# Optimization experiments

Hardware: AMD Instinct MI355X
Metric: run time of the kernel (lower is better)

The kernel has to match this reference:

```python
import jax, jax.numpy as jnp
import numpy as np

NB_HEAD = 12
INPUT_DIM = 768
HEAD_DIM = INPUT_DIM // NB_HEAD


def setup_inputs() -> dict:
    key = jax.random.key(0)
    kx, kq, kv = jax.random.split(key, 3)
    x = jax.random.normal(kx, (32, 512, INPUT_DIM), dtype=jnp.float32)
    # per-head params stacked on a leading head axis; original init: uniform(-0.1, 0.1)
    Q = jax.random.uniform(kq, (NB_HEAD, INPUT_DIM, INPUT_DIM), dtype=jnp.float32, minval=-0.1, maxval=0.1)
    V = jax.random.uniform(kv, (NB_HEAD, INPUT_DIM, HEAD_DIM), dtype=jnp.float32, minval=-0.1, maxval=0.1)
    return {"x": x, "Q": Q, "V": V}


def reference(x, Q, V):
    # x: [b, n, d]; Q: [h, d, d]; V: [h, d, e] with e = head_dim
    b, n, d = x.shape
    h = Q.shape[0]
    q = jnp.einsum('bnd,hde->bhne', x, Q)            # per-head query proj
    scores = jnp.einsum('bhne,bme->bhnm', q, x)      # QK^T with raw x as keys (no scaling)
    att = jax.nn.softmax(scores, axis=-1)            # softmax over keys
    weighted = jnp.einsum('bhnm,bmd->bhnd', att, x)  # attention-weighted values (raw x)
    out = jnp.einsum('bhnd,hde->bhne', weighted, V)  # per-head output proj
    # concat heads along feature dim (head 0 first, matching torch.cat)
    return out.transpose(0, 2, 1, 3).reshape(b, n, h * V.shape[-1])
```

## Files before the change

kernel.cpp:

```cpp
#include <hip/hip_runtime.h>
#include <stdint.h>

#define B_SZ 32
#define SEQ  512
#define DIM  768
#define NH   12
#define HD   64
#define ROWS (B_SZ*SEQ)

typedef __attribute__((ext_vector_type(4))) float f32x4;
typedef __attribute__((ext_vector_type(8))) _Float16 half8;

#define GLOAD_LDS16(gaddr, laddr) \
  __builtin_amdgcn_global_load_lds((const __attribute__((address_space(1))) void*)(gaddr), \
                                   (__attribute__((address_space(3))) void*)(laddr), 16, 0, 0)

__device__ __forceinline__ unsigned short h2u(_Float16 h){
  union { _Float16 h; unsigned short u; } c; c.h = h; return c.u;
}
__device__ __forceinline__ unsigned short f2hu(float f){
  return h2u((_Float16)f);
}

__global__ void k_split(const float* __restrict__ x,
                        unsigned short* __restrict__ xh,
                        unsigned short* __restrict__ xl, int n4){
  int i = blockIdx.x * 256 + threadIdx.x;
  if (i >= n4) return;
  float4 v = ((const float4*)x)[i];
  ushort4 h, l;
  _Float16 t;
  t = (_Float16)v.x; h.x = h2u(t); l.x = f2hu(v.x - (float)t);
  t = (_Float16)v.y; h.y = h2u(t); l.y = f2hu(v.y - (float)t);
  t = (_Float16)v.z; h.z = h2u(t); l.z = f2hu(v.z - (float)t);
  t = (_Float16)v.w; h.w = h2u(t); l.w = f2hu(v.w - (float)t);
  ((ushort4*)xh)[i] = h;
  ((ushort4*)xl)[i] = l;
}

__global__ __launch_bounds__(256) void k_transQ(const float* __restrict__ Q,
                         unsigned short* __restrict__ qth,
                         unsigned short* __restrict__ qtl){
  __shared__ float tile[32][33];
  int h = blockIdx.z;
  int d0 = blockIdx.x * 32;
  int e0 = blockIdx.y * 32;
  int tx = threadIdx.x & 31, ty = threadIdx.x >> 5;
  const float* Qh = Q + (size_t)h * DIM * DIM;
  for (int i = 0; i < 4; ++i)
    tile[ty + i*8][tx] = Qh[(size_t)(d0 + ty + i*8) * DIM + e0 + tx];
  __syncthreads();
  for (int i = 0; i < 4; ++i){
    float v = tile[tx][ty + i*8];
    size_t o = ((size_t)h * DIM + e0 + ty + i*8) * DIM + d0 + tx;
    _Float16 hi = (_Float16)v;
    qth[o] = h2u(hi);
    qtl[o] = f2hu(v - (float)hi);
  }
}

__global__ __launch_bounds__(256) void k_transV(const float* __restrict__ V,
                         unsigned short* __restrict__ vt16){
  __shared__ float tile[32][33];
  int h = blockIdx.z;
  int d0 = blockIdx.x * 32;
  int e0 = blockIdx.y * 32;
  int tx = threadIdx.x & 31, ty = threadIdx.x >> 5;
  const float* Vh = V + (size_t)h * DIM * HD;
  for (int i = 0; i < 4; ++i)
    tile[ty + i*8][tx] = Vh[(size_t)(d0 + ty + i*8) * HD + e0 + tx];
  __syncthreads();
  for (int i = 0; i < 4; ++i)
    vt16[((size_t)h * HD + e0 + ty + i*8) * DIM + d0 + tx] = f2hu(tile[tx][ty + i*8]);
}

__global__ __launch_bounds__(256) void k_gemm_xv(
    const unsigned short* __restrict__ xh,
    const unsigned short* __restrict__ vt16,
    unsigned short* __restrict__ xvT){
  __shared__ __align__(16) unsigned short lA[128*32];
  __shared__ __align__(16) unsigned short lB[64*32];
  __shared__ __align__(16) unsigned short lOut[64*128];
  int t = threadIdx.x, w = t >> 6, l = t & 63;
  int lane16 = l & 15, quad = l >> 4;
  int b = blockIdx.y, h = blockIdx.z;
  int m0 = blockIdx.x * 128;
  const unsigned short* vth = vt16 + (size_t)h * HD * DIM;
  f32x4 acc[2][4];
  for (int i = 0; i < 2; ++i) for (int j = 0; j < 4; ++j)
    for (int z = 0; z < 4; ++z) acc[i][j][z] = 0.f;

  for (int kt = 0; kt < DIM/32; ++kt){
    int k0 = kt * 32;
    __syncthreads();
    for (int rep = 0; rep < 2; ++rep){
      int id = t + rep * 256;
      int row = id >> 2, ko = (id & 3) * 8;
      GLOAD_LDS16(&xh[((size_t)(b*SEQ + m0 + row))*DIM + k0 + ko],
                  &lA[(rep*256 + w*64) * 8]);
    }
    { int row = t >> 2, ko = (t & 3) * 8;
      GLOAD_LDS16(&vth[(size_t)row*DIM + k0 + ko], &lB[(w*64) * 8]); }
    __syncthreads();
    half8 a[2];
    for (int i = 0; i < 2; ++i)
      a[i] = *(const half8*)&lA[(w*32 + i*16 + lane16)*32 + quad*8];
    for (int j = 0; j < 4; ++j){
      half8 bb = *(const half8*)&lB[(j*16 + lane16)*32 + quad*8];
      for (int i = 0; i < 2; ++i)
        acc[i][j] = __builtin_amdgcn_mfma_f32_16x16x32_f16(a[i], bb, acc[i][j], 0, 0, 0);
    }
  }
  __syncthreads();
  for (int i = 0; i < 2; ++i) for (int j = 0; j < 4; ++j) for (int r = 0; r < 4; ++r){
    int col = j*16 + lane16;
    int n  = w*32 + i*16 + quad*4 + r;
    lOut[col*128 + n] = f2hu(acc[i][j][r]);
  }
  __syncthreads();
  for (int rep = 0; rep < 4; ++rep){
    int id = t + rep*256;
    int e = id >> 4, no = (id & 15) * 8;
    *(int4*)&xvT[((size_t)(b*NH + h)*HD + e)*SEQ + m0 + no] = *(const int4*)&lOut[e*128 + no];
  }
}

__global__ __launch_bounds__(256, 2) void k_gemm_q(
    const unsigned short* __restrict__ xh, const unsigned short* __restrict__ xl,
    const unsigned short* __restrict__ bth, const unsigned short* __restrict__ btl,
    unsigned short* __restrict__ qh, unsigned short* __restrict__ ql, int ncols){
  __shared__ __align__(16) unsigned short lA[2][128*64];
  __shared__ __align__(16) unsigned short lB[2][128*64];
  int t = threadIdx.x, w = t >> 6, l = t & 63;
  int lane16 = l & 15, quad = l >> 4;
  int nlin = blockIdx.y * gridDim.x + blockIdx.x;
  int xcd = nlin & 7, jj = nlin >> 3;
  int ntc = gridDim.y;
  int m0 = (xcd * 16 + jj / ntc) * 128;
  int n0 = (jj % ntc) * 128;
  int wr = (w >> 1) * 64, wc = (w & 1) * 64;
  f32x4 acc[4][4];
  for (int i = 0; i < 4; ++i) for (int j = 0; j < 4; ++j)
    for (int z = 0; z < 4; ++z) acc[i][j][z] = 0.f;

  for (int kt = 0; kt < DIM/64; ++kt){
    int k0 = kt * 64;
    __syncthreads();
    for (int rep = 0; rep < 4; ++rep){
      int id = t + rep * 256;
      int row = id >> 3;
      int gc  = (id & 7) ^ (row & 7);
      int lb  = (rep*256 + w*64) * 8;
      size_t gA = (size_t)(m0+row)*DIM + k0 + gc*8;
      size_t gB = (size_t)(n0+row)*DIM + k0 + gc*8;
      GLOAD_LDS16(&xh [gA], &lA[0][lb]);
      GLOAD_LDS16(&xl [gA], &lA[1][lb]);
      GLOAD_LDS16(&bth[gB], &lB[0][lb]);
      GLOAD_LDS16(&btl[gB], &lB[1][lb]);
    }
    __syncthreads();
    for (int ks = 0; ks < 2; ++ks){
      int sw = ((ks*4 + quad) ^ (lane16 & 7)) * 8;
      half8 aH[4], aL[4];
      for (int i = 0; i < 4; ++i){
        int r = wr + i*16 + lane16;
        aH[i] = *(const half8*)&lA[0][r*64 + sw];
        aL[i] = *(const half8*)&lA[1][r*64 + sw];
      }
      for (int j = 0; j < 4; ++j){
        int c = wc + j*16 + lane16;
        half8 bH = *(const half8*)&lB[0][c*64 + sw];
        half8 bL = *(const half8*)&lB[1][c*64 + sw];
        for (int i = 0; i < 4; ++i){
          acc[i][j] = __builtin_amdgcn_mfma_f32_16x16x32_f16(aL[i], bH, acc[i][j], 0, 0, 0);
          acc[i][j] = __builtin_amdgcn_mfma_f32_16x16x32_f16(aH[i], bL, acc[i][j], 0, 0, 0);
          acc[i][j] = __builtin_amdgcn_mfma_f32_16x16x32_f16(aH[i], bH, acc[i][j], 0, 0, 0);
        }
      }
    }
  }
  for (int i = 0; i < 4; ++i) for (int j = 0; j < 4; ++j) for (int r = 0; r < 4; ++r){
    int row = m0 + wr + i*16 + quad*4 + r;
    int col = n0 + wc + j*16 + lane16;
    float v = acc[i][j][r];
    _Float16 hh = (_Float16)v;
    size_t o = (size_t)row*ncols + col;
    qh[o] = h2u(hh);
    ql[o] = f2hu(v - (float)hh);
  }
}

#define SEQP 520
__global__ __launch_bounds__(512) void k_attn(
    const unsigned short* __restrict__ qh, const unsigned short* __restrict__ ql,
    const unsigned short* __restrict__ xh, const unsigned short* __restrict__ xl,
    const unsigned short* __restrict__ xvT,
    float* __restrict__ out, int h0, int hc){
  __shared__ __align__(16) unsigned short lsh[73728];
  __shared__ float lStat[8*64 + 64 + 64];

  int t = threadIdx.x, w = t >> 6, l = t & 63;
  int lane16 = l & 15, quad = l >> 4;
  int nlin = blockIdx.y * gridDim.x + blockIdx.x;
  int xcd = nlin & 7, jj = nlin >> 3;
  int cpb = 8 * hc;
  int b = xcd * (B_SZ/8) + jj / cpb;
  int combo = jj % cpb;
  int hIdx = combo % hc, nt = combo / hc;
  int h = h0 + hIdx;
  int qstride = hc * DIM;
  size_t qoff = (size_t)hIdx * DIM;
  int n0 = nt * 64;
  size_t rowbase = (size_t)b * SEQ;
  const size_t dQ = (size_t)(ql - qh);
  const size_t dX = (size_t)(xl - xh);

  f32x4 accS[4][4];
  for (int i = 0; i < 4; ++i) for (int j = 0; j < 4; ++j)
    for (int z = 0; z < 4; ++z) accS[i][j][z] = 0.f;

  auto stage = [&](int kt){
    int k0 = kt * 32, bb = kt & 1;
    int qb = 65536 + bb*4096;
    {
      int row = t >> 3, s = t & 7, c = s ^ (row & 7);
      size_t hilo = (size_t)(c >> 2);
      GLOAD_LDS16(&qh[(rowbase + n0 + row)*qstride + qoff + k0 + (c & 3)*8 + hilo*dQ],
                  &lsh[qb + t*8]);
    }
    int kb = bb*32768;
    for (int rep = 0; rep < 8; ++rep){
      int id = t + rep * 512;
      int row = id >> 3, s = id & 7, c = s ^ (row & 7);
      size_t hilo = (size_t)(c >> 2);
      GLOAD_LDS16(&xh[(rowbase + row)*DIM + k0 + (c & 3)*8 + hilo*dX],
                  &lsh[kb + id*8]);
    }
  };

  stage(0);
  for (int kt = 0; kt < DIM/32; ++kt){
    __syncthreads();
    if (kt + 1 < DIM/32) stage(kt + 1);
    int bb = kt & 1;
    int qb = 65536 + bb*4096, kb = bb*32768;
    half8 aH[4], aL[4];
    for (int i = 0; i < 4; ++i){
      int r = i*16 + lane16;
      aH[i] = *(const half8*)&lsh[qb + r*64 + (( quad    ^ (r & 7))*8)];
      aL[i] = *(const half8*)&lsh[qb + r*64 + (((quad+4) ^ (r & 7))*8)];
    }
    for (int j = 0; j < 4; ++j){
      int c = w*64 + j*16 + lane16;
      half8 bH = *(const half8*)&lsh[kb + c*64 + (( quad    ^ (c & 7))*8)];
      half8 bL = *(const half8*)&lsh[kb + c*64 + (((quad+4) ^ (c & 7))*8)];
      for (int i = 0; i < 4; ++i){
        accS[i][j] = __builtin_amdgcn_mfma_f32_16x16x32_f16(aL[i], bH, accS[i][j], 0, 0, 0);
        accS[i][j] = __builtin_amdgcn_mfma_f32_16x16x32_f16(aH[i], bL, accS[i][j], 0, 0, 0);
        accS[i][j] = __builtin_amdgcn_mfma_f32_16x16x32_f16(aH[i], bH, accS[i][j], 0, 0, 0);
      }
    }
  }
  __syncthreads();

  const int XVB = 34816;
  for (int it = 0; it < 8; ++it){
    int e = it*8 + w;
    GLOAD_LDS16(&xvT[((size_t)(b*NH + h)*HD + e)*SEQ + l*8], &lsh[XVB + e*SEQP]);
  }

  float rmx[4][4];
  for (int i = 0; i < 4; ++i) for (int r = 0; r < 4; ++r){
    float m = accS[i][0][r];
    for (int j = 1; j < 4; ++j) m = fmaxf(m, accS[i][j][r]);
    for (int d = 1; d < 16; d <<= 1) m = fmaxf(m, __shfl_xor(m, d, 64));
    rmx[i][r] = m;
  }
  if (lane16 == 0)
    for (int i = 0; i < 4; ++i) for (int r = 0; r < 4; ++r)
      lStat[w*64 + i*16 + quad*4 + r] = rmx[i][r];
  __syncthreads();
  if (t < 64){
    float m = lStat[t];
    for (int ww = 1; ww < 8; ++ww) m = fmaxf(m, lStat[ww*64 + t]);
    lStat[512 + t] = m;
  }
  __syncthreads();
  float rsum[4][4];
  for (int i = 0; i < 4; ++i) for (int r = 0; r < 4; ++r){
    float g = lStat[512 + i*16 + quad*4 + r];
    float s = 0.f;
    for (int j = 0; j < 4; ++j){
      float p = __expf(accS[i][j][r] - g);
      s += p;
      lsh[(i*16 + quad*4 + r)*SEQP + (w*64 + j*16 + lane16)] = f2hu(p);
    }
    for (int d = 1; d < 16; d <<= 1) s += __shfl_xor(s, d, 64);
    rsum[i][r] = s;
  }
  if (lane16 == 0)
    for (int i = 0; i < 4; ++i) for (int r = 0; r < 4; ++r)
      lStat[w*64 + i*16 + quad*4 + r] = rsum[i][r];
  __syncthreads();
  if (t < 64){
    float s = lStat[t];
    for (int ww = 1; ww < 8; ++ww) s += lStat[ww*64 + t];
    lStat[576 + t] = s;
  }
  __syncthreads();

  f32x4 accO[4][4];
  for (int i = 0; i < 4; ++i) for (int j = 0; j < 4; ++j)
    for (int z = 0; z < 4; ++z) accO[i][j][z] = 0.f;
  for (int ks = 0; ks < 2; ++ks){
    int kb = w*64 + ks*32;
    half8 aP[4];
    for (int i = 0; i < 4; ++i)
      aP[i] = *(const half8*)&lsh[(i*16 + lane16)*SEQP + kb + quad*8];
    for (int j = 0; j < 4; ++j){
      half8 bV = *(const half8*)&lsh[XVB + (j*16 + lane16)*SEQP + kb + quad*8];
      for (int i = 0; i < 4; ++i)
        accO[i][j] = __builtin_amdgcn_mfma_f32_16x16x32_f16(aP[i], bV, accO[i][j], 0, 0, 0);
    }
  }
  __syncthreads();
  float* red = (float*)lsh;
  for (int i = 0; i < 4; ++i) for (int j = 0; j < 4; ++j) for (int r = 0; r < 4; ++r)
    red[w*4096 + (i*16 + quad*4 + r)*64 + (j*16 + lane16)] = accO[i][j][r];
  __syncthreads();
  for (int z = t; z < 4096; z += 512){
    int row = z >> 6, col = z & 63;
    float v = 0.f;
    for (int ww = 0; ww < 8; ++ww) v += red[ww*4096 + z];
    v /= lStat[576 + row];
    out[(rowbase + n0 + row)*DIM + h*HD + col] = v;
  }
}

extern "C" void kernel_launch(void* const* d_in, const int* in_sizes, int n_in,
                              void* d_out, int out_size, void* d_ws, size_t ws_size,
                              hipStream_t stream){
  const float* x = (const float*)d_in[0];
  const float* Q = (const float*)d_in[1];
  const float* V = (const float*)d_in[2];
  float* out = (float*)d_out;

  char* ws = (char*)d_ws;
  size_t off = 0;
  auto alloc = [&](size_t bytes) -> void* {
    void* p = ws + off;
    off += (bytes + 255) & ~(size_t)255;
    return p;
  };
  unsigned short* xh  = (unsigned short*)alloc((size_t)ROWS*DIM*2);
  unsigned short* xl  = (unsigned short*)alloc((size_t)ROWS*DIM*2);
  unsigned short* qth = (unsigned short*)alloc((size_t)NH*DIM*DIM*2);
  unsigned short* qtl = (unsigned short*)alloc((size_t)NH*DIM*DIM*2);
  unsigned short* vt  = (unsigned short*)alloc((size_t)NH*HD*DIM*2);
  unsigned short* xvT = (unsigned short*)alloc((size_t)B_SZ*NH*HD*SEQ*2);

  const int hcands[6] = {12, 6, 4, 3, 2, 1};
  int HC = 1;
  for (int i = 0; i < 6; ++i){
    size_t qb_bytes = ((size_t)ROWS * hcands[i] * DIM * 2 + 255) & ~(size_t)255;
    if (off + 2*qb_bytes <= ws_size){ HC = hcands[i]; break; }
  }
  unsigned short* qbh = (unsigned short*)alloc((size_t)ROWS*HC*DIM*2);
  unsigned short* qbl = (unsigned short*)alloc((size_t)ROWS*HC*DIM*2);

  int n4 = ROWS*DIM/4;
  k_split<<<n4/256, 256, 0, stream>>>(x, xh, xl, n4);
  k_transQ<<<dim3(DIM/32, DIM/32, NH), 256, 0, stream>>>(Q, qth, qtl);
  k_transV<<<dim3(DIM/32, HD/32, NH), 256, 0, stream>>>(V, vt);
  k_gemm_xv<<<dim3(4, B_SZ, NH), 256, 0, stream>>>(xh, vt, xvT);

  for (int h0 = 0; h0 < NH; h0 += HC){
    k_gemm_q<<<dim3(ROWS/128, HC*DIM/128), 256, 0, stream>>>(
        xh, xl, qth + (size_t)h0*DIM*DIM, qtl + (size_t)h0*DIM*DIM,
        qbh, qbl, HC*DIM);
    k_attn<<<dim3(8*HC, B_SZ), 512, 0, stream>>>(
        qbh, qbl, xh, xl, xvT, out, h0, HC);
  }
}
```

Before: 1.545 ms.

## Halve attention LDS footprint, drop double buffering, read values directly from global

Removes the double-buffered K/Q staging in the score loop so LDS use drops by half, allowing higher occupancy (launch bounds now request 4 waves per EU). The PV product no longer stages xvT into LDS or reduces partial sums across waves. Instead each wave owns a 32-row by 16-column output tile over the full key range and reads V fragments directly from global, with an XOR-swizzled P layout. In exchange, the score loop gains an extra barrier per step and loses overlap between loads and MFMA, relying on other resident blocks to hide latency.

```diff
diff --git a/kernel.cpp b/kernel.cpp
--- a/kernel.cpp
+++ b/kernel.cpp
@@ -190,14 +190,14 @@
   }
 }
 
-#define SEQP 520
-__global__ __launch_bounds__(512) void k_attn(
+__global__ __launch_bounds__(512, 4) void k_attn(
     const unsigned short* __restrict__ qh, const unsigned short* __restrict__ ql,
     const unsigned short* __restrict__ xh, const unsigned short* __restrict__ xl,
     const unsigned short* __restrict__ xvT,
     float* __restrict__ out, int h0, int hc){
-  __shared__ __align__(16) unsigned short lsh[73728];
+  __shared__ __align__(16) unsigned short lsh[36864];
   __shared__ float lStat[8*64 + 64 + 64];
+  const int QB = 32768;
 
   int t = threadIdx.x, w = t >> 6, l = t & 63;
   int lane16 = l & 15, quad = l >> 4;
@@ -220,40 +220,36 @@
     for (int z = 0; z < 4; ++z) accS[i][j][z] = 0.f;
 
   auto stage = [&](int kt){
-    int k0 = kt * 32, bb = kt & 1;
-    int qb = 65536 + bb*4096;
+    int k0 = kt * 32;
     {
       int row = t >> 3, s = t & 7, c = s ^ (row & 7);
       size_t hilo = (size_t)(c >> 2);
       GLOAD_LDS16(&qh[(rowbase + n0 + row)*qstride + qoff + k0 + (c & 3)*8 + hilo*dQ],
-                  &lsh[qb + t*8]);
-    }
-    int kb = bb*32768;
+                  &lsh[QB + t*8]);
+    }
     for (int rep = 0; rep < 8; ++rep){
       int id = t + rep * 512;
       int row = id >> 3, s = id & 7, c = s ^ (row & 7);
       size_t hilo = (size_t)(c >> 2);
       GLOAD_LDS16(&xh[(rowbase + row)*DIM + k0 + (c & 3)*8 + hilo*dX],
-                  &lsh[kb + id*8]);
+                  &lsh[id*8]);
     }
   };
 
-  stage(0);
   for (int kt = 0; kt < DIM/32; ++kt){
     __syncthreads();
-    if (kt + 1 < DIM/32) stage(kt + 1);
-    int bb = kt & 1;
-    int qb = 65536 + bb*4096, kb = bb*32768;
+    stage(kt);
+    __syncthreads();
     half8 aH[4], aL[4];
     for (int i = 0; i < 4; ++i){
       int r = i*16 + lane16;
-      aH[i] = *(const half8*)&lsh[qb + r*64 + (( quad    ^ (r & 7))*8)];
-      aL[i] = *(const half8*)&lsh[qb + r*64 + (((quad+4) ^ (r & 7))*8)];
+      aH[i] = *(const half8*)&lsh[QB + r*64 + (( quad    ^ (r & 7))*8)];
+      aL[i] = *(const half8*)&lsh[QB + r*64 + (((quad+4) ^ (r & 7))*8)];
     }
     for (int j = 0; j < 4; ++j){
       int c = w*64 + j*16 + lane16;
-      half8 bH = *(const half8*)&lsh[kb + c*64 + (( quad    ^ (c & 7))*8)];
-      half8 bL = *(const half8*)&lsh[kb + c*64 + (((quad+4) ^ (c & 7))*8)];
+      half8 bH = *(const half8*)&lsh[c*64 + (( quad    ^ (c & 7))*8)];
+      half8 bL = *(const half8*)&lsh[c*64 + (((quad+4) ^ (c & 7))*8)];
       for (int i = 0; i < 4; ++i){
         accS[i][j] = __builtin_amdgcn_mfma_f32_16x16x32_f16(aL[i], bH, accS[i][j], 0, 0, 0);
         accS[i][j] = __builtin_amdgcn_mfma_f32_16x16x32_f16(aH[i], bL, accS[i][j], 0, 0, 0);
@@ -262,12 +258,6 @@
     }
   }
   __syncthreads();
-
-  const int XVB = 34816;
-  for (int it = 0; it < 8; ++it){
-    int e = it*8 + w;
-    GLOAD_LDS16(&xvT[((size_t)(b*NH + h)*HD + e)*SEQ + l*8], &lsh[XVB + e*SEQP]);
-  }
 
   float rmx[4][4];
   for (int i = 0; i < 4; ++i) for (int r = 0; r < 4; ++r){
@@ -290,10 +280,13 @@
   for (int i = 0; i < 4; ++i) for (int r = 0; r < 4; ++r){
     float g = lStat[512 + i*16 + quad*4 + r];
     float s = 0.f;
+    int row = i*16 + quad*4 + r;
+    int sw = (row & 7) << 3;
     for (int j = 0; j < 4; ++j){
       float p = __expf(accS[i][j][r] - g);
       s += p;
-      lsh[(i*16 + quad*4 + r)*SEQP + (w*64 + j*16 + lane16)] = f2hu(p);
+      int key = w*64 + j*16 + lane16;
+      lsh[row*512 + (key ^ sw)] = f2hu(p);
     }
     for (int d = 1; d < 16; d <<= 1) s += __shfl_xor(s, d, 64);
     rsum[i][r] = s;
@@ -309,31 +302,22 @@
   }
   __syncthreads();
 
-  f32x4 accO[4][4];
-  for (int i = 0; i < 4; ++i) for (int j = 0; j < 4; ++j)
-    for (int z = 0; z < 4; ++z) accO[i][j][z] = 0.f;
-  for (int ks = 0; ks < 2; ++ks){
-    int kb = w*64 + ks*32;
-    half8 aP[4];
-    for (int i = 0; i < 4; ++i)
-      aP[i] = *(const half8*)&lsh[(i*16 + lane16)*SEQP + kb + quad*8];
-    for (int j = 0; j < 4; ++j){
-      half8 bV = *(const half8*)&lsh[XVB + (j*16 + lane16)*SEQP + kb + quad*8];
-      for (int i = 0; i < 4; ++i)
-        accO[i][j] = __builtin_amdgcn_mfma_f32_16x16x32_f16(aP[i], bV, accO[i][j], 0, 0, 0);
-    }
-  }
-  __syncthreads();
-  float* red = (float*)lsh;
-  for (int i = 0; i < 4; ++i) for (int j = 0; j < 4; ++j) for (int r = 0; r < 4; ++r)
-    red[w*4096 + (i*16 + quad*4 + r)*64 + (j*16 + lane16)] = accO[i][j][r];
-  __syncthreads();
-  for (int z = t; z < 4096; z += 512){
-    int row = z >> 6, col = z & 63;
-    float v = 0.f;
-    for (int ww = 0; ww < 8; ++ww) v += red[ww*4096 + z];
-    v /= lStat[576 + row];
-    out[(rowbase + n0 + row)*DIM + h*HD + col] = v;
+  int rh = (w & 1) * 32, e0 = (w >> 1) * 16;
+  f32x4 accO[2];
+  for (int i = 0; i < 2; ++i) for (int z = 0; z < 4; ++z) accO[i][z] = 0.f;
+  const unsigned short* xvp = xvT + ((size_t)(b*NH + h)*HD + e0 + lane16)*SEQ;
+  for (int ks = 0; ks < 16; ++ks){
+    int kb = ks*32;
+    half8 bV = *(const half8*)&xvp[kb + quad*8];
+    for (int i = 0; i < 2; ++i){
+      int row = rh + i*16 + lane16;
+      half8 aP = *(const half8*)&lsh[row*512 + ((kb + quad*8) ^ ((row & 7) << 3))];
+      accO[i] = __builtin_amdgcn_mfma_f32_16x16x32_f16(aP, bV, accO[i], 0, 0, 0);
+    }
+  }
+  for (int i = 0; i < 2; ++i) for (int z = 0; z < 4; ++z){
+    int row = rh + i*16 + quad*4 + z;
+    out[(rowbase + n0 + row)*DIM + h*HD + e0 + lane16] = accO[i][z] / lStat[576 + row];
   }
 }
 
```

After: 1.940 ms. +25.5%, slower.

## Process two heads per attention block to share key tile loads

Applied to the files above, without the earlier changes.

Each attention block now computes scores for a pair of heads, loading each key (x) tile into LDS once and reusing it for both heads' QK^T MFMAs. The softmax and PV phases then run sequentially per head. This halves the key-tile global traffic and block count, at the cost of doubled score accumulators (heavy register pressure), an extra barrier per k-step because the Q staging is no longer double-buffered, and a launch bound of two blocks per CU. The head-chunk candidates are restricted to even values, so the 12-head case falls back to 6.

```diff
diff --git a/kernel.cpp b/kernel.cpp
--- a/kernel.cpp
+++ b/kernel.cpp
@@ -191,7 +191,7 @@
 }
 
 #define SEQP 520
-__global__ __launch_bounds__(512) void k_attn(
+__global__ __launch_bounds__(512, 2) void k_attn(
     const unsigned short* __restrict__ qh, const unsigned short* __restrict__ ql,
     const unsigned short* __restrict__ xh, const unsigned short* __restrict__ xl,
     const unsigned short* __restrict__ xvT,
@@ -203,32 +203,24 @@
   int lane16 = l & 15, quad = l >> 4;
   int nlin = blockIdx.y * gridDim.x + blockIdx.x;
   int xcd = nlin & 7, jj = nlin >> 3;
-  int cpb = 8 * hc;
+  int hp = hc >> 1;
+  int cpb = 8 * hp;
   int b = xcd * (B_SZ/8) + jj / cpb;
   int combo = jj % cpb;
-  int hIdx = combo % hc, nt = combo / hc;
-  int h = h0 + hIdx;
+  int pIdx = combo % hp, nt = combo / hp;
   int qstride = hc * DIM;
-  size_t qoff = (size_t)hIdx * DIM;
+  size_t qoff0 = (size_t)(2*pIdx) * DIM;
   int n0 = nt * 64;
   size_t rowbase = (size_t)b * SEQ;
   const size_t dQ = (size_t)(ql - qh);
   const size_t dX = (size_t)(xl - xh);
 
-  f32x4 accS[4][4];
+  f32x4 accS0[4][4], accS1[4][4];
   for (int i = 0; i < 4; ++i) for (int j = 0; j < 4; ++j)
-    for (int z = 0; z < 4; ++z) accS[i][j][z] = 0.f;
-
-  auto stage = [&](int kt){
-    int k0 = kt * 32, bb = kt & 1;
-    int qb = 65536 + bb*4096;
-    {
-      int row = t >> 3, s = t & 7, c = s ^ (row & 7);
-      size_t hilo = (size_t)(c >> 2);
-      GLOAD_LDS16(&qh[(rowbase + n0 + row)*qstride + qoff + k0 + (c & 3)*8 + hilo*dQ],
-                  &lsh[qb + t*8]);
-    }
-    int kb = bb*32768;
+    for (int z = 0; z < 4; ++z){ accS0[i][j][z] = 0.f; accS1[i][j][z] = 0.f; }
+
+  auto stage_keys = [&](int kt){
+    int k0 = kt * 32, kb = (kt & 1) * 32768;
     for (int rep = 0; rep < 8; ++rep){
       int id = t + rep * 512;
       int row = id >> 3, s = id & 7, c = s ^ (row & 7);
@@ -237,104 +229,148 @@
                   &lsh[kb + id*8]);
     }
   };
-
-  stage(0);
+  auto stage_q = [&](int kt){
+    int k0 = kt * 32;
+    int row = t >> 3, s = t & 7, c = s ^ (row & 7);
+    size_t hilo = (size_t)(c >> 2);
+    size_t g = (rowbase + n0 + row)*(size_t)qstride + qoff0 + k0 + (c & 3)*8 + hilo*dQ;
+    GLOAD_LDS16(&qh[g],       &lsh[65536 + t*8]);
+    GLOAD_LDS16(&qh[g + DIM], &lsh[65536 + 4096 + t*8]);
+  };
+
+  stage_keys(0);
   for (int kt = 0; kt < DIM/32; ++kt){
     __syncthreads();
-    if (kt + 1 < DIM/32) stage(kt + 1);
-    int bb = kt & 1;
-    int qb = 65536 + bb*4096, kb = bb*32768;
-    half8 aH[4], aL[4];
-    for (int i = 0; i < 4; ++i){
-      int r = i*16 + lane16;
-      aH[i] = *(const half8*)&lsh[qb + r*64 + (( quad    ^ (r & 7))*8)];
-      aL[i] = *(const half8*)&lsh[qb + r*64 + (((quad+4) ^ (r & 7))*8)];
-    }
-    for (int j = 0; j < 4; ++j){
-      int c = w*64 + j*16 + lane16;
-      half8 bH = *(const half8*)&lsh[kb + c*64 + (( quad    ^ (c & 7))*8)];
-      half8 bL = *(const half8*)&lsh[kb + c*64 + (((quad+4) ^ (c & 7))*8)];
+    stage_q(kt);
+    __syncthreads();
+    if (kt + 1 < DIM/32) stage_keys(kt + 1);
+    int kb = (kt & 1) * 32768;
+    {
+      half8 aH[4], aL[4];
+      #pragma unroll
       for (int i = 0; i < 4; ++i){
-        accS[i][j] = __builtin_amdgcn_mfma_f32_16x16x32_f16(aL[i], bH, accS[i][j], 0, 0, 0);
-        accS[i][j] = __builtin_amdgcn_mfma_f32_16x16x32_f16(aH[i], bL, accS[i][j], 0, 0, 0);
-        accS[i][j] = __builtin_amdgcn_mfma_f32_16x16x32_f16(aH[i], bH, accS[i][j], 0, 0, 0);
+        int r = i*16 + lane16;
+        aH[i] = *(const half8*)&lsh[65536 + r*64 + (( quad    ^ (r & 7))*8)];
+        aL[i] = *(const half8*)&lsh[65536 + r*64 + (((quad+4) ^ (r & 7))*8)];
+      }
+      #pragma unroll
+      for (int j = 0; j < 4; ++j){
+        int c = w*64 + j*16 + lane16;
+        half8 bH = *(const half8*)&lsh[kb + c*64 + (( quad    ^ (c & 7))*8)];
+        half8 bL = *(const half8*)&lsh[kb + c*64 + (((quad+4) ^ (c & 7))*8)];
+        #pragma unroll
+        for (int i = 0; i < 4; ++i){
+          accS0[i][j] = __builtin_amdgcn_mfma_f32_16x16x32_f16(aL[i], bH, accS0[i][j], 0, 0, 0);
+          accS0[i][j] = __builtin_amdgcn_mfma_f32_16x16x32_f16(aH[i], bL, accS0[i][j], 0, 0, 0);
+          accS0[i][j] = __builtin_amdgcn_mfma_f32_16x16x32_f16(aH[i], bH, accS0[i][j], 0, 0, 0);
+        }
+      }
+    }
+    {
+      half8 aH[4], aL[4];
+      #pragma unroll
+      for (int i = 0; i < 4; ++i){
+        int r = i*16 + lane16;
+        aH[i] = *(const half8*)&lsh[65536 + 4096 + r*64 + (( quad    ^ (r & 7))*8)];
+        aL[i] = *(const half8*)&lsh[65536 + 4096 + r*64 + (((quad+4) ^ (r & 7))*8)];
+      }
+      #pragma unroll
+      for (int j = 0; j < 4; ++j){
+        int c = w*64 + j*16 + lane16;
+        half8 bH = *(const half8*)&lsh[kb + c*64 + (( quad    ^ (c & 7))*8)];
+        half8 bL = *(const half8*)&lsh[kb + c*64 + (((quad+4) ^ (c & 7))*8)];
+        #pragma unroll
+        for (int i = 0; i < 4; ++i){
+          accS1[i][j] = __builtin_amdgcn_mfma_f32_16x16x32_f16(aL[i], bH, accS1[i][j], 0, 0, 0);
+          accS1[i][j] = __builtin_amdgcn_mfma_f32_16x16x32_f16(aH[i], bL, accS1[i][j], 0, 0, 0);
+          accS1[i][j] = __builtin_amdgcn_mfma_f32_16x16x32_f16(aH[i], bH, accS1[i][j], 0, 0, 0);
+        }
       }
     }
   }
   __syncthreads();
 
   const int XVB = 34816;
-  for (int it = 0; it < 8; ++it){
-    int e = it*8 + w;
-    GLOAD_LDS16(&xvT[((size_t)(b*NH + h)*HD + e)*SEQ + l*8], &lsh[XVB + e*SEQP]);
-  }
-
-  float rmx[4][4];
-  for (int i = 0; i < 4; ++i) for (int r = 0; r < 4; ++r){
-    float m = accS[i][0][r];
-    for (int j = 1; j < 4; ++j) m = fmaxf(m, accS[i][j][r]);
-    for (int d = 1; d < 16; d <<= 1) m = fmaxf(m, __shfl_xor(m, d, 64));
-    rmx[i][r] = m;
-  }
-  if (lane16 == 0)
-    for (int i = 0; i < 4; ++i) for (int r = 0; r < 4; ++r)
-      lStat[w*64 + i*16 + quad*4 + r] = rmx[i][r];
-  __syncthreads();
-  if (t < 64){
-    float m = lStat[t];
-    for (int ww = 1; ww < 8; ++ww) m = fmaxf(m, lStat[ww*64 + t]);
-    lStat[512 + t] = m;
-  }
-  __syncthreads();
-  float rsum[4][4];
-  for (int i = 0; i < 4; ++i) for (int r = 0; r < 4; ++r){
-    float g = lStat[512 + i*16 + quad*4 + r];
-    float s = 0.f;
-    for (int j = 0; j < 4; ++j){
-      float p = __expf(accS[i][j][r] - g);
-      s += p;
-      lsh[(i*16 + quad*4 + r)*SEQP + (w*64 + j*16 + lane16)] = f2hu(p);
-    }
-    for (int d = 1; d < 16; d <<= 1) s += __shfl_xor(s, d, 64);
-    rsum[i][r] = s;
-  }
-  if (lane16 == 0)
-    for (int i = 0; i < 4; ++i) for (int r = 0; r < 4; ++r)
-      lStat[w*64 + i*16 + quad*4 + r] = rsum[i][r];
-  __syncthreads();
-  if (t < 64){
-    float s = lStat[t];
-    for (int ww = 1; ww < 8; ++ww) s += lStat[ww*64 + t];
-    lStat[576 + t] = s;
-  }
-  __syncthreads();
-
-  f32x4 accO[4][4];
-  for (int i = 0; i < 4; ++i) for (int j = 0; j < 4; ++j)
-    for (int z = 0; z < 4; ++z) accO[i][j][z] = 0.f;
-  for (int ks = 0; ks < 2; ++ks){
-    int kb = w*64 + ks*32;
-    half8 aP[4];
-    for (int i = 0; i < 4; ++i)
-      aP[i] = *(const half8*)&lsh[(i*16 + lane16)*SEQP + kb + quad*8];
-    for (int j = 0; j < 4; ++j){
-      half8 bV = *(const half8*)&lsh[XVB + (j*16 + lane16)*SEQP + kb + quad*8];
+  auto p23 = [&](f32x4 (&accS)[4][4], int myh){
+    for (int it = 0; it < 8; ++it){
+      int e = it*8 + w;
+      GLOAD_LDS16(&xvT[((size_t)(b*NH + myh)*HD + e)*SEQ + l*8], &lsh[XVB + e*SEQP]);
+    }
+    float rmx[4][4];
+    #pragma unroll
+    for (int i = 0; i < 4; ++i) for (int r = 0; r < 4; ++r){
+      float m = accS[i][0][r];
+      for (int j = 1; j < 4; ++j) m = fmaxf(m, accS[i][j][r]);
+      for (int d = 1; d < 16; d <<= 1) m = fmaxf(m, __shfl_xor(m, d, 64));
+      rmx[i][r] = m;
+    }
+    if (lane16 == 0)
+      for (int i = 0; i < 4; ++i) for (int r = 0; r < 4; ++r)
+        lStat[w*64 + i*16 + quad*4 + r] = rmx[i][r];
+    __syncthreads();
+    if (t < 64){
+      float m = lStat[t];
+      for (int ww = 1; ww < 8; ++ww) m = fmaxf(m, lStat[ww*64 + t]);
+      lStat[512 + t] = m;
+    }
+    __syncthreads();
+    float rsum[4][4];
+    #pragma unroll
+    for (int i = 0; i < 4; ++i) for (int r = 0; r < 4; ++r){
+      float g = lStat[512 + i*16 + quad*4 + r];
+      float s = 0.f;
+      for (int j = 0; j < 4; ++j){
+        float p = __expf(accS[i][j][r] - g);
+        s += p;
+        lsh[(i*16 + quad*4 + r)*SEQP + (w*64 + j*16 + lane16)] = f2hu(p);
+      }
+      for (int d = 1; d < 16; d <<= 1) s += __shfl_xor(s, d, 64);
+      rsum[i][r] = s;
+    }
+    if (lane16 == 0)
+      for (int i = 0; i < 4; ++i) for (int r = 0; r < 4; ++r)
+        lStat[w*64 + i*16 + quad*4 + r] = rsum[i][r];
+    __syncthreads();
+    if (t < 64){
+      float s = lStat[t];
+      for (int ww = 1; ww < 8; ++ww) s += lStat[ww*64 + t];
+      lStat[576 + t] = s;
+    }
+    __syncthreads();
+
+    f32x4 accO[4][4];
+    for (int i = 0; i < 4; ++i) for (int j = 0; j < 4; ++j)
+      for (int z = 0; z < 4; ++z) accO[i][j][z] = 0.f;
+    for (int ks = 0; ks < 2; ++ks){
+      int kb = w*64 + ks*32;
+      half8 aP[4];
+      #pragma unroll
       for (int i = 0; i < 4; ++i)
-        accO[i][j] = __builtin_amdgcn_mfma_f32_16x16x32_f16(aP[i], bV, accO[i][j], 0, 0, 0);
-    }
-  }
-  __syncthreads();
-  float* red = (float*)lsh;
-  for (int i = 0; i < 4; ++i) for (int j = 0; j < 4; ++j) for (int r = 0; r < 4; ++r)
-    red[w*4096 + (i*16 + quad*4 + r)*64 + (j*16 + lane16)] = accO[i][j][r];
-  __syncthreads();
-  for (int z = t; z < 4096; z += 512){
-    int row = z >> 6, col = z & 63;
-    float v = 0.f;
-    for (int ww = 0; ww < 8; ++ww) v += red[ww*4096 + z];
-    v /= lStat[576 + row];
-    out[(rowbase + n0 + row)*DIM + h*HD + col] = v;
-  }
+        aP[i] = *(const half8*)&lsh[(i*16 + lane16)*SEQP + kb + quad*8];
+      #pragma unroll
+      for (int j = 0; j < 4; ++j){
+        half8 bV = *(const half8*)&lsh[XVB + (j*16 + lane16)*SEQP + kb + quad*8];
+        for (int i = 0; i < 4; ++i)
+          accO[i][j] = __builtin_amdgcn_mfma_f32_16x16x32_f16(aP[i], bV, accO[i][j], 0, 0, 0);
+      }
+    }
+    __syncthreads();
+    float* red = (float*)lsh;
+    for (int i = 0; i < 4; ++i) for (int j = 0; j < 4; ++j) for (int r = 0; r < 4; ++r)
+      red[w*4096 + (i*16 + quad*4 + r)*64 + (j*16 + lane16)] = accO[i][j][r];
+    __syncthreads();
+    for (int z = t; z < 4096; z += 512){
+      int row = z >> 6, col = z & 63;
+      float v = 0.f;
+      for (int ww = 0; ww < 8; ++ww) v += red[ww*4096 + z];
+      v /= lStat[576 + row];
+      out[(rowbase + n0 + row)*DIM + myh*HD + col] = v;
+    }
+    __syncthreads();
+  };
+
+  p23(accS0, h0 + 2*pIdx);
+  p23(accS1, h0 + 2*pIdx + 1);
 }
 
 extern "C" void kernel_launch(void* const* d_in, const int* in_sizes, int n_in,
@@ -359,9 +395,9 @@
   unsigned short* vt  = (unsigned short*)alloc((size_t)NH*HD*DIM*2);
   unsigned short* xvT = (unsigned short*)alloc((size_t)B_SZ*NH*HD*SEQ*2);
 
-  const int hcands[6] = {12, 6, 4, 3, 2, 1};
-  int HC = 1;
-  for (int i = 0; i < 6; ++i){
+  const int hcands[3] = {6, 4, 2};
+  int HC = 2;
+  for (int i = 0; i < 3; ++i){
     size_t qb_bytes = ((size_t)ROWS * hcands[i] * DIM * 2 + 255) & ~(size_t)255;
     if (off + 2*qb_bytes <= ws_size){ HC = hcands[i]; break; }
   }
@@ -378,7 +414,7 @@
     k_gemm_q<<<dim3(ROWS/128, HC*DIM/128), 256, 0, stream>>>(
         xh, xl, qth + (size_t)h0*DIM*DIM, qtl + (size_t)h0*DIM*DIM,
         qbh, qbl, HC*DIM);
-    k_attn<<<dim3(8*HC, B_SZ), 512, 0, stream>>>(
+    k_attn<<<dim3(8*(HC/2), B_SZ), 512, 0, stream>>>(
         qbh, qbl, xh, xl, xvT, out, h0, HC);
   }
 }
```

New measurement: 1.284 ms. 1.2x faster.
